# Kernel tuning notes

Measured on AMD Instinct MI355X. Metric: run time of the kernel, lower is better.

## Reference

```python
import jax, jax.numpy as jnp
import numpy as np

N, D_IN, D_OUT, H = 8192, 256, 128, 2
SLOPE = 0.2
EPS = 1e-5  # InstanceNorm2d default eps


def setup_inputs() -> dict:
    key = jax.random.key(0)
    ks = jax.random.split(key, 6)
    x = jax.random.normal(ks[0], (N, D_IN), dtype=jnp.float32)
    conn_mask = jnp.where(jax.random.uniform(ks[1], (N, N)) < 0.05, 0.0, -1e9).astype(jnp.float32)
    W = jax.random.normal(ks[2], (H, D_IN, D_OUT), dtype=jnp.float32) * 0.05
    a_src = jax.random.normal(ks[3], (H, D_OUT), dtype=jnp.float32) * 0.1
    a_tgt = jax.random.normal(ks[4], (H, D_OUT), dtype=jnp.float32) * 0.1
    W_res = jax.random.normal(ks[5], (D_OUT, D_IN), dtype=jnp.float32) * 0.05
    return {"x": x, "conn_mask": conn_mask, "W": W, "a_src": a_src, "a_tgt": a_tgt, "W_res": W_res}


def reference(x, conn_mask, W, a_src, a_tgt, W_res):
    # dropout is identity in eval mode
    proj = jnp.einsum('nd,hdf->hnf', x, W)                      # [H,N,F]
    s_src = jnp.einsum('hnf,hf->hn', proj, a_src)[:, :, None]   # [H,N,1]
    s_tgt = jnp.einsum('hnf,hf->hn', proj, a_tgt)[:, None, :]   # [H,1,N]
    scores = jax.nn.leaky_relu(s_src + s_tgt, negative_slope=SLOPE)  # [H,N,N]
    attn = jax.nn.softmax(conn_mask[None] + scores, axis=1)     # softmax over dim=1 as in torch code
    vals = jnp.einsum('hmn,hnf->hmf', attn, proj)               # bmm -> [H,N,F]
    vals = vals.mean(axis=0)                                    # head mean -> [N,F]
    # InstanceNorm2d(1, affine=False) over the whole [N,F] plane, biased variance
    mu = vals.mean()
    var = jnp.mean(jnp.square(vals - mu))
    vals_norm = (vals - mu) / jnp.sqrt(var + EPS)
    out = vals_norm + x @ W_res.T                               # residual projection (no bias)
    out = jax.nn.elu(out)
    return (out, conn_mask)
```

## Files before the change

### kernel.cpp

```cpp
#include <hip/hip_runtime.h>
#include <stdint.h>

#define NN   8192
#define DIN  256
#define FF   128
#define NF   (NN*FF)
#define SLOPE 0.2f
#define EPSI  1e-5f

typedef float vf4 __attribute__((ext_vector_type(4)));
typedef short bf16x8 __attribute__((ext_vector_type(8)));
typedef float f32x4 __attribute__((ext_vector_type(4)));

#define OFF_PROJ   0
#define OFF_RESID  (2*NF)
#define OFF_PACKED (3*NF)
#define OFF_SS     (4*NF)
#define OFF_ST     (OFF_SS + 2*NN)
#define OFF_CSUM   (OFF_ST + 2*NN)
#define OFF_STATS  (OFF_CSUM + 2*NN)
#define OFF_NTAB   (OFF_STATS + 16)
#define OFF_VALS   (OFF_NTAB + 4*NN)
#define OFF_WT     (OFF_VALS + NF)
#define OFF_PT2    (OFF_WT + DIN*FF)
#define OFF_VPART  (OFF_PT2 + NF)

__device__ __forceinline__ float lrelu(float x) { return x >= 0.f ? x : SLOPE * x; }

__device__ __forceinline__ uint32_t bfpack(float a, float b) {
  uint32_t ua = __float_as_uint(a); ua += 0x7fffu + ((ua >> 16) & 1u);
  uint32_t ub = __float_as_uint(b); ub += 0x7fffu + ((ub >> 16) & 1u);
  return (ua >> 16) | (ub & 0xffff0000u);
}

__global__ __launch_bounds__(256) void k_wt(const float* __restrict__ wres, float* __restrict__ wt) {
  int i = blockIdx.x * 256 + threadIdx.x;
  int d = i >> 7, f = i & 127;
  wt[i] = wres[f * DIN + d];
}

__global__ __launch_bounds__(256) void k_gemm(const float* __restrict__ x, const float* __restrict__ Wh,
                                              const float* __restrict__ wt, float* __restrict__ proj,
                                              float* __restrict__ resid) {
  const int h = blockIdx.y;
  const float* __restrict__ Wsrc = (h < 2) ? (Wh + h * (DIN * FF)) : wt;
  float* __restrict__ outp = (h < 2) ? (proj + h * NF) : resid;
  const int row0 = blockIdx.x * 64;
  __shared__ float xs[64 * 68];
  const int tid = threadIdx.x;
  const int ft = tid & 15, rt = tid >> 4;
  const int f0 = ft * 8, r0 = rt * 4;
  float acc[4][8];
#pragma unroll
  for (int j = 0; j < 4; ++j)
#pragma unroll
    for (int k = 0; k < 8; ++k) acc[j][k] = 0.f;

  for (int kc = 0; kc < 4; ++kc) {
    const int d0 = kc * 64;
#pragma unroll
    for (int k2 = 0; k2 < 4; ++k2) {
      int i = tid * 4 + k2 * 1024;
      int r = i >> 6, dd = i & 63;
      *(float4*)&xs[r * 68 + dd] = *(const float4*)&x[(row0 + r) * DIN + d0 + dd];
    }
    __syncthreads();
#pragma unroll
    for (int g = 0; g < 16; ++g) {
      const int dd = g * 4;
      float xr[4][4];
#pragma unroll
      for (int j = 0; j < 4; ++j) {
        float4 t = *(const float4*)&xs[(r0 + j) * 68 + dd];
        xr[j][0] = t.x; xr[j][1] = t.y; xr[j][2] = t.z; xr[j][3] = t.w;
      }
#pragma unroll
      for (int i = 0; i < 4; ++i) {
        float4 wa = *(const float4*)&Wsrc[(d0 + dd + i) * FF + f0];
        float4 wb = *(const float4*)&Wsrc[(d0 + dd + i) * FF + f0 + 4];
#pragma unroll
        for (int j = 0; j < 4; ++j) {
          float xx = xr[j][i];
          acc[j][0] += xx * wa.x; acc[j][1] += xx * wa.y; acc[j][2] += xx * wa.z; acc[j][3] += xx * wa.w;
          acc[j][4] += xx * wb.x; acc[j][5] += xx * wb.y; acc[j][6] += xx * wb.z; acc[j][7] += xx * wb.w;
        }
      }
    }
    __syncthreads();
  }
#pragma unroll
  for (int j = 0; j < 4; ++j) {
    int row = row0 + r0 + j;
    *(float4*)&outp[row * FF + f0]     = make_float4(acc[j][0], acc[j][1], acc[j][2], acc[j][3]);
    *(float4*)&outp[row * FF + f0 + 4] = make_float4(acc[j][4], acc[j][5], acc[j][6], acc[j][7]);
  }
}

__global__ __launch_bounds__(256) void k_sprep(const float* __restrict__ proj, const float* __restrict__ a_src,
                                               const float* __restrict__ a_tgt, float* __restrict__ ss,
                                               float* __restrict__ st, uint32_t* __restrict__ packed) {
  int lane = threadIdx.x & 63, wid = threadIdx.x >> 6;
  int n = blockIdx.x * 4 + wid;
  float2 q0 = *(const float2*)&proj[n * FF + 2 * lane];
  float2 q1 = *(const float2*)&proj[NF + n * FF + 2 * lane];
  float2 as0 = *(const float2*)&a_src[2 * lane];
  float2 at0 = *(const float2*)&a_tgt[2 * lane];
  float2 as1 = *(const float2*)&a_src[FF + 2 * lane];
  float2 at1 = *(const float2*)&a_tgt[FF + 2 * lane];
  float v0 = q0.x * as0.x + q0.y * as0.y;
  float v1 = q0.x * at0.x + q0.y * at0.y;
  float v2 = q1.x * as1.x + q1.y * as1.y;
  float v3 = q1.x * at1.x + q1.y * at1.y;
#pragma unroll
  for (int o = 1; o < 64; o <<= 1) {
    v0 += __shfl_xor(v0, o); v1 += __shfl_xor(v1, o);
    v2 += __shfl_xor(v2, o); v3 += __shfl_xor(v3, o);
  }
  uint2 pk;
  pk.x = bfpack(q0.x, q1.x);
  pk.y = bfpack(q0.y, q1.y);
  *(uint2*)&packed[n * FF + 2 * lane] = pk;
  if (lane == 0) { ss[n] = v0; ss[NN + n] = v2; st[n] = v1; st[NN + n] = v3; }
}

__global__ __launch_bounds__(256) void k_tpose(const uint32_t* __restrict__ packed, uint32_t* __restrict__ pt2) {
  __shared__ uint32_t sb[32][129];
  const int t = threadIdx.x, c = blockIdx.x;
  const int nl = t >> 3, fb = (t & 7) * 16;
#pragma unroll
  for (int i = 0; i < 4; ++i) {
    uint4 v = *(const uint4*)&packed[(c * 32 + nl) * FF + fb + i * 4];
    sb[nl][fb + i * 4] = v.x; sb[nl][fb + i * 4 + 1] = v.y;
    sb[nl][fb + i * 4 + 2] = v.z; sb[nl][fb + i * 4 + 3] = v.w;
  }
  __syncthreads();
  const int h = t >> 7, f = t & 127;
  uint32_t wbuf[16];
#pragma unroll
  for (int p = 0; p < 16; ++p) {
    uint32_t a = sb[2 * p][f], b = sb[2 * p + 1][f];
    wbuf[p] = h ? ((a >> 16) | (b & 0xffff0000u)) : ((a & 0xffffu) | (b << 16));
  }
  uint32_t* dst = pt2 + ((c * 2 + h) * 128 + f) * 16;
#pragma unroll
  for (int i = 0; i < 4; ++i)
    *(uint4*)&dst[i * 4] = make_uint4(wbuf[i * 4], wbuf[i * 4 + 1], wbuf[i * 4 + 2], wbuf[i * 4 + 3]);
}

__global__ __launch_bounds__(256) void k_scan(const float* __restrict__ mask, float* __restrict__ maskout,
                                              const float* __restrict__ ss, const float* __restrict__ st,
                                              float* __restrict__ csum, uint32_t* __restrict__ bitmask) {
  const int tid = threadIdx.x;
  const int lane = tid & 63, wv = tid >> 6;
  const int n = blockIdx.x * 256 + tid;
  const int m0 = blockIdx.y * 128;
  const int wbase = blockIdx.x * 8 + wv * 2;
  const float st0 = st[n], st1 = st[NN + n];
  const float ssA = ss[m0 + lane],      ssB = ss[m0 + 64 + lane];
  const float ssC = ss[NN + m0 + lane], ssD = ss[NN + m0 + 64 + lane];
  float c0 = 0.f, c1 = 0.f;

  for (int i = 0; i < 128; i += 8) {
    float v[8];
#pragma unroll
    for (int r = 0; r < 8; ++r)
      v[r] = __builtin_nontemporal_load(&mask[(size_t)(m0 + i + r) * NN + n]);
#pragma unroll
    for (int r = 0; r < 8; ++r) {
      const int m = m0 + i + r;
      __builtin_nontemporal_store(v[r], &maskout[(size_t)m * NN + n]);
      bool e = v[r] > -0.5e9f;
      unsigned long long bm = __ballot(e);
      if (lane == 0)
        *(uint2*)&bitmask[m * 256 + wbase] = make_uint2((uint32_t)bm, (uint32_t)(bm >> 32));
      const int ri = i + r;
      float s0 = __uint_as_float(__builtin_amdgcn_readlane(
                   __float_as_uint(ri < 64 ? ssA : ssB), ri & 63));
      float s1 = __uint_as_float(__builtin_amdgcn_readlane(
                   __float_as_uint(ri < 64 ? ssC : ssD), ri & 63));
      float w0 = __expf(lrelu(s0 + st0));
      float w1 = __expf(lrelu(s1 + st1));
      c0 += e ? w0 : 0.f;
      c1 += e ? w1 : 0.f;
    }
  }
  atomicAdd(&csum[n], c0);
  atomicAdd(&csum[NN + n], c1);
}

__global__ __launch_bounds__(256) void k_ntab(const float* __restrict__ st, const float* __restrict__ csum,
                                              float4* __restrict__ ntab) {
  int i = blockIdx.x * 256 + threadIdx.x;
  ntab[i] = make_float4(st[i], st[NN + i], 1.f / csum[i], 1.f / csum[NN + i]);
}

__global__ __launch_bounds__(128) void k_vals(const uint32_t* __restrict__ bitmask, const uint32_t* __restrict__ pt2,
                                              const float4* __restrict__ ntab, const float* __restrict__ ss,
                                              float* __restrict__ vpart) {
  __shared__ short B2[2][8][4][16][8];
  __shared__ short A2[2][4][4][16][8];
  const int t = threadIdx.x;
  const int lane = t & 63, wid = t >> 6;
  const int m0 = blockIdx.x * 64;
  const int nc = blockIdx.y;
  const int q = lane >> 4, col = lane & 15;
  const int n2 = t & 15, mg = t >> 4;

  float ssm0[8], ssm1[8];
#pragma unroll
  for (int p = 0; p < 8; ++p) {
    ssm0[p] = ss[m0 + mg + 8 * p];
    ssm1[p] = ss[NN + m0 + mg + 8 * p];
  }

  f32x4 acc[2][8];
#pragma unroll
  for (int i = 0; i < 2; ++i)
#pragma unroll
    for (int j = 0; j < 8; ++j) acc[i][j] = (f32x4){0.f, 0.f, 0.f, 0.f};

  uint32_t* B2w = (uint32_t*)&B2[0][0][0][0][0];
  uint32_t* A2w = (uint32_t*)&A2[0][0][0][0][0];

  for (int s = 0; s < 32; ++s) {
    const int n0 = nc * 1024 + s * 32;
    const uint32_t* src = pt2 + (nc * 32 + s) * 4096;
#pragma unroll
    for (int h = 0; h < 2; ++h) {
      const uint4* p4 = (const uint4*)&src[(h * 128 + t) * 16];
#pragma unroll
      for (int k = 0; k < 4; ++k) {
        uint4 v = p4[k];
        *(uint4*)&B2w[(((h * 8 + (t >> 4)) * 4 + k) * 16 + (t & 15)) * 4] = v;
      }
    }
    float4 na = ntab[n0 + 2 * n2];
    float4 nb = ntab[n0 + 2 * n2 + 1];
#pragma unroll
    for (int p = 0; p < 8; ++p) {
      const int ml = mg + 8 * p;
      const int mt = ml >> 4, mcol = ml & 15;
      uint32_t bw = bitmask[(size_t)(m0 + ml) * 256 + (n0 >> 5)];
      float e0a = __expf(lrelu(ssm0[p] + na.x)) * na.z;
      float e1a = __expf(lrelu(ssm1[p] + na.y)) * na.w;
      float e0b = __expf(lrelu(ssm0[p] + nb.x)) * nb.z;
      float e1b = __expf(lrelu(ssm1[p] + nb.y)) * nb.w;
      bool b0 = (bw >> (2 * n2)) & 1, b1 = (bw >> (2 * n2 + 1)) & 1;
      e0a = b0 ? e0a : 0.f; e1a = b0 ? e1a : 0.f;
      e0b = b1 ? e0b : 0.f; e1b = b1 ? e1b : 0.f;
      int base = (mt * 4 + (n2 >> 2)) * 64 + mcol * 4 + (n2 & 3);
      A2w[base] = bfpack(e0a, e0b);
      A2w[base + 1024] = bfpack(e1a, e1b);
    }
    __syncthreads();
    bf16x8 a00 = *(const bf16x8*)&A2[0][wid * 2][q][col][0];
    bf16x8 a01 = *(const bf16x8*)&A2[0][wid * 2 + 1][q][col][0];
    bf16x8 a10 = *(const bf16x8*)&A2[1][wid * 2][q][col][0];
    bf16x8 a11 = *(const bf16x8*)&A2[1][wid * 2 + 1][q][col][0];
#pragma unroll
    for (int ft = 0; ft < 8; ++ft) {
      bf16x8 b0 = *(const bf16x8*)&B2[0][ft][q][col][0];
      acc[0][ft] = __builtin_amdgcn_mfma_f32_16x16x32_bf16(a00, b0, acc[0][ft], 0, 0, 0);
      acc[1][ft] = __builtin_amdgcn_mfma_f32_16x16x32_bf16(a01, b0, acc[1][ft], 0, 0, 0);
      bf16x8 b1 = *(const bf16x8*)&B2[1][ft][q][col][0];
      acc[0][ft] = __builtin_amdgcn_mfma_f32_16x16x32_bf16(a10, b1, acc[0][ft], 0, 0, 0);
      acc[1][ft] = __builtin_amdgcn_mfma_f32_16x16x32_bf16(a11, b1, acc[1][ft], 0, 0, 0);
    }
    __syncthreads();
  }

  float* dst = vpart + (size_t)nc * NF;
#pragma unroll
  for (int mt2 = 0; mt2 < 2; ++mt2)
#pragma unroll
    for (int ft = 0; ft < 8; ++ft)
#pragma unroll
      for (int r = 0; r < 4; ++r) {
        int mrow = m0 + (wid * 2 + mt2) * 16 + q * 4 + r;
        dst[mrow * FF + ft * 16 + col] = 0.5f * acc[mt2][ft][r];
      }
}

__global__ __launch_bounds__(256) void k_stats(const float* __restrict__ vpart, float* __restrict__ vals,
                                               float* __restrict__ stats) {
  int i = (blockIdx.x * 256 + threadIdx.x) * 4;
  float4 a = make_float4(0.f, 0.f, 0.f, 0.f);
#pragma unroll
  for (int p = 0; p < 8; ++p) {
    float4 v = *(const float4*)&vpart[(size_t)p * NF + i];
    a.x += v.x; a.y += v.y; a.z += v.z; a.w += v.w;
  }
  *(float4*)&vals[i] = a;
  float s = a.x + a.y + a.z + a.w;
  float q = a.x * a.x + a.y * a.y + a.z * a.z + a.w * a.w;
#pragma unroll
  for (int o = 1; o < 64; o <<= 1) { s += __shfl_xor(s, o); q += __shfl_xor(q, o); }
  if ((threadIdx.x & 63) == 0) { atomicAdd(stats, s); atomicAdd(stats + 1, q); }
}

__global__ __launch_bounds__(256) void k_final(const float* __restrict__ vals, const float* __restrict__ resid,
                                               const float* __restrict__ stats, float* __restrict__ out) {
  int i = (blockIdx.x * 256 + threadIdx.x) * 4;
  float mu = stats[0] * (1.f / NF);
  float var = stats[1] * (1.f / NF) - mu * mu;
  float rs = rsqrtf(var + EPSI);
  float4 v = *(const float4*)&vals[i];
  float4 r = *(const float4*)&resid[i];
  float t0 = (v.x - mu) * rs + r.x;
  float t1 = (v.y - mu) * rs + r.y;
  float t2 = (v.z - mu) * rs + r.z;
  float t3 = (v.w - mu) * rs + r.w;
  float4 o;
  o.x = t0 > 0.f ? t0 : expm1f(t0);
  o.y = t1 > 0.f ? t1 : expm1f(t1);
  o.z = t2 > 0.f ? t2 : expm1f(t2);
  o.w = t3 > 0.f ? t3 : expm1f(t3);
  *(float4*)&out[i] = o;
}

extern "C" void kernel_launch(void* const* d_in, const int* in_sizes, int n_in,
                              void* d_out, int out_size, void* d_ws, size_t ws_size,
                              hipStream_t stream) {
  const float* x     = (const float*)d_in[0];
  const float* mask  = (const float*)d_in[1];
  const float* W     = (const float*)d_in[2];
  const float* a_src = (const float*)d_in[3];
  const float* a_tgt = (const float*)d_in[4];
  const float* wres  = (const float*)d_in[5];
  float* out = (float*)d_out;
  float* wsf = (float*)d_ws;

  float*    proj    = wsf + OFF_PROJ;
  uint32_t* bitmask = (uint32_t*)(wsf + OFF_PROJ);
  float*    resid   = wsf + OFF_RESID;
  uint32_t* packed  = (uint32_t*)(wsf + OFF_PACKED);
  float*    ss      = wsf + OFF_SS;
  float*    st      = wsf + OFF_ST;
  float*    csum    = wsf + OFF_CSUM;
  float*    stats   = wsf + OFF_STATS;
  float4*   ntab    = (float4*)(wsf + OFF_NTAB);
  float*    vals    = wsf + OFF_VALS;
  float*    wt      = wsf + OFF_WT;
  uint32_t* pt2     = (uint32_t*)(wsf + OFF_PT2);
  float*    vpart   = wsf + OFF_VPART;

  (void)hipMemsetAsync(csum, 0, (2 * NN + 16) * sizeof(float), stream);

  hipLaunchKernelGGL(k_wt,    dim3(DIN * FF / 256), dim3(256), 0, stream, wres, wt);
  hipLaunchKernelGGL(k_gemm,  dim3(NN / 64, 3),     dim3(256), 0, stream, x, W, wt, proj, resid);
  hipLaunchKernelGGL(k_sprep, dim3(NN / 4),         dim3(256), 0, stream, proj, a_src, a_tgt, ss, st, packed);
  hipLaunchKernelGGL(k_tpose, dim3(NN / 32),        dim3(256), 0, stream, packed, pt2);
  hipLaunchKernelGGL(k_scan,  dim3(NN / 256, NN / 128), dim3(256), 0, stream, mask, out + NF, ss, st, csum, bitmask);
  hipLaunchKernelGGL(k_ntab,  dim3(NN / 256),       dim3(256), 0, stream, st, csum, ntab);
  hipLaunchKernelGGL(k_vals,  dim3(NN / 64, 8),     dim3(128), 0, stream, bitmask, pt2, ntab, ss, vpart);
  hipLaunchKernelGGL(k_stats, dim3(NF / 1024),      dim3(256), 0, stream, vpart, vals, stats);
  hipLaunchKernelGGL(k_final, dim3(NF / 1024),      dim3(256), 0, stream, vals, resid, stats, out);
}
```

Before: 721.3 us.

## Enlarge attention-value tiles to 128 rows, halve GEMM tiles, use exp2 intrinsic

The attention-value kernel now uses 256 threads over 128 target rows per block. This lets each streamed projection tile in shared memory be reused by twice as many rows, and each thread loads half of it instead of looping over both heads. The projection GEMM shrinks to 32-row tiles with 4-column thread outputs, which doubles the block count for better occupancy at the cost of more repeated weight reads. Exponentials switch to the native exp2 instruction, with the scores prescaled by log2(e), removing a multiply per exp. This may change rounding slightly.

```diff
diff --git a/kernel.cpp b/kernel.cpp
--- a/kernel.cpp
+++ b/kernel.cpp
@@ -7,6 +7,7 @@
 #define NF   (NN*FF)
 #define SLOPE 0.2f
 #define EPSI  1e-5f
+#define LOG2E 1.4426950408889634f
 
 typedef float vf4 __attribute__((ext_vector_type(4)));
 typedef short bf16x8 __attribute__((ext_vector_type(8)));
@@ -27,6 +28,8 @@
 
 __device__ __forceinline__ float lrelu(float x) { return x >= 0.f ? x : SLOPE * x; }
 
+__device__ __forceinline__ float exp2fast(float x) { return __builtin_amdgcn_exp2f(x); }
+
 __device__ __forceinline__ uint32_t bfpack(float a, float b) {
   uint32_t ua = __float_as_uint(a); ua += 0x7fffu + ((ua >> 16) & 1u);
   uint32_t ub = __float_as_uint(b); ub += 0x7fffu + ((ub >> 16) & 1u);
@@ -45,21 +48,21 @@
   const int h = blockIdx.y;
   const float* __restrict__ Wsrc = (h < 2) ? (Wh + h * (DIN * FF)) : wt;
   float* __restrict__ outp = (h < 2) ? (proj + h * NF) : resid;
-  const int row0 = blockIdx.x * 64;
-  __shared__ float xs[64 * 68];
+  const int row0 = blockIdx.x * 32;
+  __shared__ float xs[32 * 68];
   const int tid = threadIdx.x;
-  const int ft = tid & 15, rt = tid >> 4;
-  const int f0 = ft * 8, r0 = rt * 4;
-  float acc[4][8];
+  const int ft = tid & 31, rt = tid >> 5;
+  const int f0 = ft * 4, r0 = rt * 4;
+  float acc[4][4];
 #pragma unroll
   for (int j = 0; j < 4; ++j)
 #pragma unroll
-    for (int k = 0; k < 8; ++k) acc[j][k] = 0.f;
+    for (int k = 0; k < 4; ++k) acc[j][k] = 0.f;
 
   for (int kc = 0; kc < 4; ++kc) {
     const int d0 = kc * 64;
 #pragma unroll
-    for (int k2 = 0; k2 < 4; ++k2) {
+    for (int k2 = 0; k2 < 2; ++k2) {
       int i = tid * 4 + k2 * 1024;
       int r = i >> 6, dd = i & 63;
       *(float4*)&xs[r * 68 + dd] = *(const float4*)&x[(row0 + r) * DIN + d0 + dd];
@@ -76,13 +79,12 @@
       }
 #pragma unroll
       for (int i = 0; i < 4; ++i) {
-        float4 wa = *(const float4*)&Wsrc[(d0 + dd + i) * FF + f0];
-        float4 wb = *(const float4*)&Wsrc[(d0 + dd + i) * FF + f0 + 4];
+        float4 w = *(const float4*)&Wsrc[(d0 + dd + i) * FF + f0];
 #pragma unroll
         for (int j = 0; j < 4; ++j) {
           float xx = xr[j][i];
-          acc[j][0] += xx * wa.x; acc[j][1] += xx * wa.y; acc[j][2] += xx * wa.z; acc[j][3] += xx * wa.w;
-          acc[j][4] += xx * wb.x; acc[j][5] += xx * wb.y; acc[j][6] += xx * wb.z; acc[j][7] += xx * wb.w;
+          acc[j][0] += xx * w.x; acc[j][1] += xx * w.y;
+          acc[j][2] += xx * w.z; acc[j][3] += xx * w.w;
         }
       }
     }
@@ -91,8 +93,7 @@
 #pragma unroll
   for (int j = 0; j < 4; ++j) {
     int row = row0 + r0 + j;
-    *(float4*)&outp[row * FF + f0]     = make_float4(acc[j][0], acc[j][1], acc[j][2], acc[j][3]);
-    *(float4*)&outp[row * FF + f0 + 4] = make_float4(acc[j][4], acc[j][5], acc[j][6], acc[j][7]);
+    *(float4*)&outp[row * FF + f0] = make_float4(acc[j][0], acc[j][1], acc[j][2], acc[j][3]);
   }
 }
 
@@ -155,9 +156,9 @@
   const int n = blockIdx.x * 256 + tid;
   const int m0 = blockIdx.y * 128;
   const int wbase = blockIdx.x * 8 + wv * 2;
-  const float st0 = st[n], st1 = st[NN + n];
-  const float ssA = ss[m0 + lane],      ssB = ss[m0 + 64 + lane];
-  const float ssC = ss[NN + m0 + lane], ssD = ss[NN + m0 + 64 + lane];
+  const float st0 = st[n] * LOG2E, st1 = st[NN + n] * LOG2E;
+  const float ssA = ss[m0 + lane] * LOG2E,      ssB = ss[m0 + 64 + lane] * LOG2E;
+  const float ssC = ss[NN + m0 + lane] * LOG2E, ssD = ss[NN + m0 + 64 + lane] * LOG2E;
   float c0 = 0.f, c1 = 0.f;
 
   for (int i = 0; i < 128; i += 8) {
@@ -178,8 +179,8 @@
                    __float_as_uint(ri < 64 ? ssA : ssB), ri & 63));
       float s1 = __uint_as_float(__builtin_amdgcn_readlane(
                    __float_as_uint(ri < 64 ? ssC : ssD), ri & 63));
-      float w0 = __expf(lrelu(s0 + st0));
-      float w1 = __expf(lrelu(s1 + st1));
+      float w0 = exp2fast(lrelu(s0 + st0));
+      float w1 = exp2fast(lrelu(s1 + st1));
       c0 += e ? w0 : 0.f;
       c1 += e ? w1 : 0.f;
     }
@@ -191,26 +192,27 @@
 __global__ __launch_bounds__(256) void k_ntab(const float* __restrict__ st, const float* __restrict__ csum,
                                               float4* __restrict__ ntab) {
   int i = blockIdx.x * 256 + threadIdx.x;
-  ntab[i] = make_float4(st[i], st[NN + i], 1.f / csum[i], 1.f / csum[NN + i]);
-}
-
-__global__ __launch_bounds__(128) void k_vals(const uint32_t* __restrict__ bitmask, const uint32_t* __restrict__ pt2,
+  ntab[i] = make_float4(st[i] * LOG2E, st[NN + i] * LOG2E, 1.f / csum[i], 1.f / csum[NN + i]);
+}
+
+__global__ __launch_bounds__(256) void k_vals(const uint32_t* __restrict__ bitmask, const uint32_t* __restrict__ pt2,
                                               const float4* __restrict__ ntab, const float* __restrict__ ss,
                                               float* __restrict__ vpart) {
   __shared__ short B2[2][8][4][16][8];
-  __shared__ short A2[2][4][4][16][8];
+  __shared__ short A2[2][8][4][16][8];
   const int t = threadIdx.x;
   const int lane = t & 63, wid = t >> 6;
-  const int m0 = blockIdx.x * 64;
+  const int m0 = blockIdx.x * 128;
   const int nc = blockIdx.y;
   const int q = lane >> 4, col = lane & 15;
   const int n2 = t & 15, mg = t >> 4;
+  const int fr = t & 127, hB = t >> 7;
 
   float ssm0[8], ssm1[8];
 #pragma unroll
   for (int p = 0; p < 8; ++p) {
-    ssm0[p] = ss[m0 + mg + 8 * p];
-    ssm1[p] = ss[NN + m0 + mg + 8 * p];
+    ssm0[p] = ss[m0 + mg + 16 * p] * LOG2E;
+    ssm1[p] = ss[NN + m0 + mg + 16 * p] * LOG2E;
   }
 
   f32x4 acc[2][8];
@@ -225,32 +227,30 @@
   for (int s = 0; s < 32; ++s) {
     const int n0 = nc * 1024 + s * 32;
     const uint32_t* src = pt2 + (nc * 32 + s) * 4096;
-#pragma unroll
-    for (int h = 0; h < 2; ++h) {
-      const uint4* p4 = (const uint4*)&src[(h * 128 + t) * 16];
+    {
+      const uint4* p4 = (const uint4*)&src[t * 16];
 #pragma unroll
       for (int k = 0; k < 4; ++k) {
         uint4 v = p4[k];
-        *(uint4*)&B2w[(((h * 8 + (t >> 4)) * 4 + k) * 16 + (t & 15)) * 4] = v;
+        *(uint4*)&B2w[(((hB * 8 + (fr >> 4)) * 4 + k) * 16 + (fr & 15)) * 4] = v;
       }
     }
     float4 na = ntab[n0 + 2 * n2];
     float4 nb = ntab[n0 + 2 * n2 + 1];
 #pragma unroll
     for (int p = 0; p < 8; ++p) {
-      const int ml = mg + 8 * p;
-      const int mt = ml >> 4, mcol = ml & 15;
+      const int ml = mg + 16 * p;
       uint32_t bw = bitmask[(size_t)(m0 + ml) * 256 + (n0 >> 5)];
-      float e0a = __expf(lrelu(ssm0[p] + na.x)) * na.z;
-      float e1a = __expf(lrelu(ssm1[p] + na.y)) * na.w;
-      float e0b = __expf(lrelu(ssm0[p] + nb.x)) * nb.z;
-      float e1b = __expf(lrelu(ssm1[p] + nb.y)) * nb.w;
+      float e0a = exp2fast(lrelu(ssm0[p] + na.x)) * na.z;
+      float e1a = exp2fast(lrelu(ssm1[p] + na.y)) * na.w;
+      float e0b = exp2fast(lrelu(ssm0[p] + nb.x)) * nb.z;
+      float e1b = exp2fast(lrelu(ssm1[p] + nb.y)) * nb.w;
       bool b0 = (bw >> (2 * n2)) & 1, b1 = (bw >> (2 * n2 + 1)) & 1;
       e0a = b0 ? e0a : 0.f; e1a = b0 ? e1a : 0.f;
       e0b = b1 ? e0b : 0.f; e1b = b1 ? e1b : 0.f;
-      int base = (mt * 4 + (n2 >> 2)) * 64 + mcol * 4 + (n2 & 3);
+      int base = (p * 4 + (n2 >> 2)) * 64 + mg * 4 + (n2 & 3);
       A2w[base] = bfpack(e0a, e0b);
-      A2w[base + 1024] = bfpack(e1a, e1b);
+      A2w[base + 2048] = bfpack(e1a, e1b);
     }
     __syncthreads();
     bf16x8 a00 = *(const bf16x8*)&A2[0][wid * 2][q][col][0];
@@ -347,12 +347,12 @@
   (void)hipMemsetAsync(csum, 0, (2 * NN + 16) * sizeof(float), stream);
 
   hipLaunchKernelGGL(k_wt,    dim3(DIN * FF / 256), dim3(256), 0, stream, wres, wt);
-  hipLaunchKernelGGL(k_gemm,  dim3(NN / 64, 3),     dim3(256), 0, stream, x, W, wt, proj, resid);
+  hipLaunchKernelGGL(k_gemm,  dim3(NN / 32, 3),     dim3(256), 0, stream, x, W, wt, proj, resid);
   hipLaunchKernelGGL(k_sprep, dim3(NN / 4),         dim3(256), 0, stream, proj, a_src, a_tgt, ss, st, packed);
   hipLaunchKernelGGL(k_tpose, dim3(NN / 32),        dim3(256), 0, stream, packed, pt2);
   hipLaunchKernelGGL(k_scan,  dim3(NN / 256, NN / 128), dim3(256), 0, stream, mask, out + NF, ss, st, csum, bitmask);
   hipLaunchKernelGGL(k_ntab,  dim3(NN / 256),       dim3(256), 0, stream, st, csum, ntab);
-  hipLaunchKernelGGL(k_vals,  dim3(NN / 64, 8),     dim3(128), 0, stream, bitmask, pt2, ntab, ss, vpart);
+  hipLaunchKernelGGL(k_vals,  dim3(NN / 128, 8),    dim3(256), 0, stream, bitmask, pt2, ntab, ss, vpart);
   hipLaunchKernelGGL(k_stats, dim3(NF / 1024),      dim3(256), 0, stream, vpart, vals, stats);
   hipLaunchKernelGGL(k_final, dim3(NF / 1024),      dim3(256), 0, stream, vals, resid, stats, out);
 }
```

Result: faster. 706.2 us (-2.1%).
